# Kernel tuning notes

Measured on AMD Instinct MI355X. Metric: run time of the kernel, lower is better.

The kernel has to match this reference:

```python
import jax, jax.numpy as jnp
import numpy as np

B, N, C = 2, 2048, 768
H = 12
HD = C // H  # 64


def setup_inputs() -> dict:
    key = jax.random.key(0)
    ks = jax.random.split(key, 6)
    s = 0.02
    x = jax.random.normal(ks[0], (B, N, C), dtype=jnp.float32)
    xpos = jnp.arange(B * N, dtype=jnp.int64).reshape(B, N) % N
    W_qkv = jax.random.normal(ks[1], (3 * C, C), dtype=jnp.float32) * s
    b_qkv = jnp.zeros((3 * C,), dtype=jnp.float32)
    W_proj = jax.random.normal(ks[2], (C, C), dtype=jnp.float32) * s
    b_proj = jnp.zeros((C,), dtype=jnp.float32)
    return {"x": x, "xpos": xpos, "W_qkv": W_qkv, "b_qkv": b_qkv,
            "W_proj": W_proj, "b_proj": b_proj}


def reference(x, xpos, W_qkv, b_qkv, W_proj, b_proj):
    # rope is None in this configuration -> xpos is unused, matching torch module.
    Bx, Nx, Cx = x.shape
    scale = (Cx // H) ** -0.5
    qkv = x @ W_qkv.T + b_qkv                     # [B, N, 3C]
    qkv = qkv.reshape(Bx, Nx, 3, H, HD)
    q = jnp.einsum('bnhd->bhnd', qkv[:, :, 0])    # [B, H, N, HD]
    k = jnp.einsum('bnhd->bhnd', qkv[:, :, 1])
    v = jnp.einsum('bnhd->bhnd', qkv[:, :, 2])
    attn = jnp.einsum('bhnd,bhmd->bhnm', q, k) * scale  # [B, H, N, N]
    attn = jax.nn.softmax(attn, axis=-1)
    out = jnp.einsum('bhnm,bhmd->bhnd', attn, v)  # [B, H, N, HD]
    out = jnp.einsum('bhnd->bnhd', out).reshape(Bx, Nx, Cx)
    return out @ W_proj.T + b_proj
```

## Files before the change

kernel.cpp:

```cpp
#include <hip/hip_runtime.h>
#include <hip/hip_bf16.h>


typedef _Float16 half8 __attribute__((ext_vector_type(8)));
typedef _Float16 half4_t __attribute__((ext_vector_type(4)));
typedef float floatx4 __attribute__((ext_vector_type(4)));
typedef float floatx16 __attribute__((ext_vector_type(16)));
typedef unsigned int uintx4 __attribute__((ext_vector_type(4)));
typedef unsigned int uintx2 __attribute__((ext_vector_type(2)));

#define SCALE_LOG2E 0.1803368801111204f

constexpr int XH_OFF    = 0;
constexpr int WQKV_OFF  = XH_OFF + 4096 * 768;
constexpr int WPROJ_OFF = WQKV_OFF + 2304 * 768;
constexpr int QK_OFF    = WPROJ_OFF + 768 * 768;
constexpr int VTH_OFF   = QK_OFF + 4096 * 1536;
constexpr int PO_OFF    = VTH_OFF + 24 * 64 * 2048;
constexpr int PSTAT_OFF = PO_OFF + 2 * 24 * 2048 * 64;

__device__ __forceinline__ void gl16(const _Float16* g, _Float16* l) {
  __builtin_amdgcn_global_load_lds(
      (const __attribute__((address_space(1))) unsigned int*)g,
      (__attribute__((address_space(3))) unsigned int*)l, 16, 0, 0);
}

__global__ __launch_bounds__(256) void cvt_all(const float* __restrict__ x,
                                               const float* __restrict__ wqkv,
                                               const float* __restrict__ wproj,
                                               _Float16* __restrict__ ws) {
  constexpr int n1 = 4096 * 768 / 4;
  constexpr int n2 = 2304 * 768 / 4;
  int i = blockIdx.x * 256 + threadIdx.x;
  const float* src; _Float16* dst; int j;
  if (i < n1)           { src = x;     dst = ws + XH_OFF;    j = i; }
  else if (i < n1 + n2) { src = wqkv;  dst = ws + WQKV_OFF;  j = i - n1; }
  else                  { src = wproj; dst = ws + WPROJ_OFF; j = i - n1 - n2; }
  floatx4 f = *(const floatx4*)(src + 4 * j);
  half4_t h;
  h[0] = (_Float16)f[0]; h[1] = (_Float16)f[1];
  h[2] = (_Float16)f[2]; h[3] = (_Float16)f[3];
  *(half4_t*)(dst + 4 * j) = h;
}

__global__ __launch_bounds__(256) void qkv_gemm(const _Float16* __restrict__ xh,
                                                const _Float16* __restrict__ wh,
                                                const float* __restrict__ bias,
                                                _Float16* __restrict__ qkh,
                                                _Float16* __restrict__ vth) {
  __shared__ __align__(16) _Float16 sA[128 * 64];
  __shared__ __align__(16) _Float16 sB[128 * 64];
  const int tid = threadIdx.x;
  const int nblk = blockIdx.x % 18, mblk = blockIdx.x / 18;
  const int lane = tid & 63, w = tid >> 6;
  const int lane15 = lane & 15, quad = lane >> 4;
  const int lrow = lane >> 3, lchunk = lane & 7;
  const int wq = w >> 1, wn = w & 1;

  floatx4 acc[4][4];
#pragma unroll
  for (int mt = 0; mt < 4; ++mt)
#pragma unroll
    for (int nt = 0; nt < 4; ++nt) acc[mt][nt] = (floatx4){0.f, 0.f, 0.f, 0.f};

  for (int kt = 0; kt < 12; ++kt) {
    if (kt) __syncthreads();
#pragma unroll
    for (int i = 0; i < 8; ++i) {
      int g = i * 32 + w * 8;
      if (g < 128)
        gl16(xh + (mblk * 128 + g + lrow) * 768 + kt * 64 + lchunk * 8, sA + g * 64);
      else
        gl16(wh + (nblk * 128 + (g - 128) + lrow) * 768 + kt * 64 + lchunk * 8,
             sB + (g - 128) * 64);
    }
    __syncthreads();
#pragma unroll
    for (int ks = 0; ks < 2; ++ks) {
      half8 af[4], bf[4];
#pragma unroll
      for (int mt = 0; mt < 4; ++mt)
        af[mt] = *(const half8*)(sA + (wq * 64 + mt * 16 + lane15) * 64 + ks * 32 + quad * 8);
#pragma unroll
      for (int nt = 0; nt < 4; ++nt)
        bf[nt] = *(const half8*)(sB + (wn * 64 + nt * 16 + lane15) * 64 + ks * 32 + quad * 8);
#pragma unroll
      for (int mt = 0; mt < 4; ++mt)
#pragma unroll
        for (int nt = 0; nt < 4; ++nt)
          acc[mt][nt] = __builtin_amdgcn_mfma_f32_16x16x32_f16(af[mt], bf[nt], acc[mt][nt], 0, 0, 0);
    }
  }

  const int mbase = mblk * 128 + wq * 64;
#pragma unroll
  for (int nt = 0; nt < 4; ++nt) {
    int cbase = nblk * 128 + wn * 64 + nt * 16;
    float bv = bias[cbase + lane15];
    if (cbase < 1536) {
      int col = cbase + lane15;
      float sc = (cbase < 768) ? SCALE_LOG2E : 1.0f;
#pragma unroll
      for (int mt = 0; mt < 4; ++mt)
#pragma unroll
        for (int r = 0; r < 4; ++r) {
          int token = mbase + mt * 16 + quad * 4 + r;
          qkh[token * 1536 + col] = (_Float16)((acc[mt][nt][r] + bv) * sc);
        }
    } else {
      int dcol = cbase - 1536 + lane15;
      int h = dcol >> 6, d = dcol & 63;
#pragma unroll
      for (int mt = 0; mt < 4; ++mt) {
        int tok0 = mbase + mt * 16 + quad * 4;
        int b = tok0 >> 11, n0 = tok0 & 2047;
        int bh = b * 12 + h;
        half4_t hv;
#pragma unroll
        for (int r = 0; r < 4; ++r) hv[r] = (_Float16)(acc[mt][nt][r] + bv);
        *(half4_t*)(vth + (bh * 64 + d) * 2048 + n0) = hv;
      }
    }
  }
}

__global__ __launch_bounds__(256, 4) void attn_fused(const _Float16* __restrict__ qkh,
                                                     const _Float16* __restrict__ vth,
                                                     _Float16* __restrict__ pO,
                                                     float* __restrict__ pL) {
  __shared__ __align__(16) _Float16 sK[2][64 * 64];
  __shared__ __align__(16) _Float16 sVT[2][64 * 64];
  const int tid = threadIdx.x;
  const int bx = blockIdx.x;
  const int bh = bx % 24;
  const int rest = bx / 24;
  const int ks = rest & 1, qt = rest >> 1;
  const int b = bh / 12, h = bh % 12;
  const int lane = tid & 63, w = tid >> 6;
  const int q = lane & 31, hi = lane >> 5;

  const int qkbase = b * 2048 * 1536 + h * 64;
  const int qrow = qt * 128 + w * 32 + q;

  half8 qf[4];
#pragma unroll
  for (int c = 0; c < 4; ++c)
    qf[c] = *(const half8*)(qkh + qkbase + qrow * 1536 + c * 16 + hi * 8);

  const int l3 = lane >> 3;
  const int lc = (lane & 7) ^ l3;
  const int key0 = ks * 1024;
  const _Float16* kbase = qkh + qkbase + 768 + (key0 + w * 8 + l3) * 1536 + lc * 8;
  const _Float16* vbase = vth + (bh * 64 + w * 8 + l3) * 2048 + key0 + lc * 8;

  floatx16 O[2];
#pragma unroll
  for (int dg = 0; dg < 2; ++dg)
#pragma unroll
    for (int i = 0; i < 16; ++i) O[dg][i] = 0.f;
  float lrow = 0.f;

  auto stage = [&](int kt, int bufsel) {
    _Float16* dK = (_Float16*)sK[bufsel] + w * 512;
    _Float16* dV = (_Float16*)sVT[bufsel] + w * 512;
    const _Float16* kc = kbase + kt * 64 * 1536;
    const _Float16* vc = vbase + kt * 64;
    gl16(kc, dK);
    gl16(kc + 32 * 1536, dK + 2048);
    gl16(vc, dV);
    gl16(vc + 32 * 2048, dV + 2048);
  };

  stage(0, 0);

  for (int kt = 0; kt < 16; ++kt) {
    __syncthreads();
    if (kt < 15) stage(kt + 1, (kt + 1) & 1);
    const _Float16* cK = &sK[kt & 1][0];
    const _Float16* cV = &sVT[kt & 1][0];

    float rsum = 0.f;
#pragma unroll
    for (int og = 0; og < 2; ++og) {
      floatx16 s;
#pragma unroll
      for (int i = 0; i < 16; ++i) s[i] = 0.f;
      const int krow = og * 32 + q;
#pragma unroll
      for (int c = 0; c < 4; ++c) {
        half8 kf = *(const half8*)(cK + krow * 64 + (((c * 2 + hi) ^ (krow & 7)) * 8));
        s = __builtin_amdgcn_mfma_f32_32x32x16_f16(kf, qf[c], s, 0, 0, 0);
      }

#pragma unroll
      for (int mm = 0; mm < 2; ++mm) {
        const int rb = mm * 8;
        float e0 = __builtin_amdgcn_exp2f(s[rb + 0]);
        float e1 = __builtin_amdgcn_exp2f(s[rb + 1]);
        float e2 = __builtin_amdgcn_exp2f(s[rb + 2]);
        float e3 = __builtin_amdgcn_exp2f(s[rb + 3]);
        float e4 = __builtin_amdgcn_exp2f(s[rb + 4]);
        float e5 = __builtin_amdgcn_exp2f(s[rb + 5]);
        float e6 = __builtin_amdgcn_exp2f(s[rb + 6]);
        float e7 = __builtin_amdgcn_exp2f(s[rb + 7]);
        rsum += ((e0 + e1) + (e2 + e3)) + ((e4 + e5) + (e6 + e7));
        unsigned ua = __builtin_bit_cast(unsigned, __builtin_amdgcn_cvt_pkrtz(e0, e1));
        unsigned ub = __builtin_bit_cast(unsigned, __builtin_amdgcn_cvt_pkrtz(e2, e3));
        unsigned uc = __builtin_bit_cast(unsigned, __builtin_amdgcn_cvt_pkrtz(e4, e5));
        unsigned ud = __builtin_bit_cast(unsigned, __builtin_amdgcn_cvt_pkrtz(e6, e7));
        uintx2 sAC = __builtin_amdgcn_permlane32_swap(ua, uc, false, false);
        uintx2 sBD = __builtin_amdgcn_permlane32_swap(ub, ud, false, false);
        uintx4 u; u[0] = sAC[0]; u[1] = sBD[0]; u[2] = sAC[1]; u[3] = sBD[1];
        half8 bfrag = __builtin_bit_cast(half8, u);

        const int rc2 = (og * 2 + mm) * 2 + hi;
#pragma unroll
        for (int dg = 0; dg < 2; ++dg) {
          const int vrow = dg * 32 + q;
          half8 vf = *(const half8*)(cV + vrow * 64 + ((rc2 ^ (vrow & 7)) * 8));
          O[dg] = __builtin_amdgcn_mfma_f32_32x32x16_f16(vf, bfrag, O[dg], 0, 0, 0);
        }
      }
    }
    lrow += rsum;
  }

  const int prow = (ks * 24 + bh) * 2048 + qt * 128 + w * 32;
#pragma unroll
  for (int dg = 0; dg < 2; ++dg)
#pragma unroll
    for (int g2 = 0; g2 < 4; ++g2) {
      half4_t hv;
#pragma unroll
      for (int e = 0; e < 4; ++e) hv[e] = (_Float16)O[dg][g2 * 4 + e];
      *(half4_t*)(pO + (prow + q) * 64 + dg * 32 + g2 * 8 + hi * 4) = hv;
    }
  lrow += __shfl_xor(lrow, 32, 64);
  if (lane < 32) pL[prow + lane] = lrow;
}

__global__ __launch_bounds__(256) void proj_gemm(const _Float16* __restrict__ pO,
                                                 const float* __restrict__ pL,
                                                 const _Float16* __restrict__ wh,
                                                 const float* __restrict__ bias,
                                                 float* __restrict__ out) {
  __shared__ __align__(16) _Float16 sA[64 * 72];
  __shared__ __align__(16) _Float16 sB[128 * 64];
  const int tid = threadIdx.x;
  const int nblk = blockIdx.x % 6, mblk = blockIdx.x / 6;
  const int lane = tid & 63, w = tid >> 6;
  const int lane15 = lane & 15, quad = lane >> 4;
  const int lrow = lane >> 3, lchunk = lane & 7;
  const int arow = tid >> 2, achk = tid & 3;
  const int tok0 = mblk * 64;
  const int b = tok0 >> 11, tokl = tok0 & 2047;

  floatx4 acc[4][2];
#pragma unroll
  for (int mt = 0; mt < 4; ++mt)
#pragma unroll
    for (int nt = 0; nt < 2; ++nt) acc[mt][nt] = (floatx4){0.f, 0.f, 0.f, 0.f};

  for (int kt = 0; kt < 12; ++kt) {
    const int bh = b * 12 + kt;
    const int row1 = bh * 2048 + tokl + arow;
    const int row2 = (24 + bh) * 2048 + tokl + arow;
    float f = 1.0f / (pL[row1] + pL[row2]);

    if (kt) __syncthreads();
#pragma unroll
    for (int i = 0; i < 4; ++i) {
      int g = w * 32 + 8 * i;
      gl16(wh + (nblk * 128 + g + lrow) * 768 + kt * 64 + lchunk * 8, sB + g * 64);
    }
#pragma unroll
    for (int cc = 0; cc < 2; ++cc) {
      int c8 = achk + 4 * cc;
      half8 o1 = *(const half8*)(pO + row1 * 64 + c8 * 8);
      half8 o2 = *(const half8*)(pO + row2 * 64 + c8 * 8);
      half8 o;
#pragma unroll
      for (int e = 0; e < 8; ++e)
        o[e] = (_Float16)(f * ((float)o1[e] + (float)o2[e]));
      *(half8*)(sA + arow * 72 + c8 * 8) = o;
    }
    __syncthreads();

#pragma unroll
    for (int ksplit = 0; ksplit < 2; ++ksplit) {
      half8 af[4], bf[2];
#pragma unroll
      for (int mt = 0; mt < 4; ++mt)
        af[mt] = *(const half8*)(sA + (mt * 16 + lane15) * 72 + ksplit * 32 + quad * 8);
#pragma unroll
      for (int nt = 0; nt < 2; ++nt)
        bf[nt] = *(const half8*)(sB + (w * 32 + nt * 16 + lane15) * 64 + ksplit * 32 + quad * 8);
#pragma unroll
      for (int mt = 0; mt < 4; ++mt)
#pragma unroll
        for (int nt = 0; nt < 2; ++nt)
          acc[mt][nt] = __builtin_amdgcn_mfma_f32_16x16x32_f16(af[mt], bf[nt], acc[mt][nt], 0, 0, 0);
    }
  }

  const int mbase = mblk * 64;
#pragma unroll
  for (int nt = 0; nt < 2; ++nt) {
    int col = nblk * 128 + w * 32 + nt * 16 + lane15;
    float bv = bias[col];
#pragma unroll
    for (int mt = 0; mt < 4; ++mt)
#pragma unroll
      for (int r = 0; r < 4; ++r) {
        int token = mbase + mt * 16 + quad * 4 + r;
        out[token * 768 + col] = acc[mt][nt][r] + bv;
      }
  }
}

extern "C" void kernel_launch(void* const* d_in, const int* in_sizes, int n_in,
                              void* d_out, int out_size, void* d_ws, size_t ws_size,
                              hipStream_t stream) {
  const float* x     = (const float*)d_in[0];
  const float* wqkv  = (const float*)d_in[2];
  const float* bqkv  = (const float*)d_in[3];
  const float* wproj = (const float*)d_in[4];
  const float* bproj = (const float*)d_in[5];
  float* out = (float*)d_out;

  _Float16* ws = (_Float16*)d_ws;
  _Float16* xh     = ws + XH_OFF;
  _Float16* wqkvh  = ws + WQKV_OFF;
  _Float16* wprojh = ws + WPROJ_OFF;
  _Float16* qkh    = ws + QK_OFF;
  _Float16* vth    = ws + VTH_OFF;
  _Float16* pO     = ws + PO_OFF;
  float*    pL     = (float*)(ws + PSTAT_OFF);

  constexpr int total_v4 = (4096 * 768 + 2304 * 768 + 768 * 768) / 4;
  cvt_all<<<total_v4 / 256, 256, 0, stream>>>(x, wqkv, wproj, ws);
  qkv_gemm<<<32 * 18, 256, 0, stream>>>(xh, wqkvh, bqkv, qkh, vth);
  attn_fused<<<24 * 32, 256, 0, stream>>>(qkh, vth, pO, pL);
  proj_gemm<<<64 * 6, 256, 0, stream>>>(pO, pL, wprojh, bproj, out);
}
```

Measured before the change: 165.3 us.

## Switch QKV and projection GEMMs to 32x32x16 MFMA with XOR-swizzled LDS

Both the QKV and output-projection GEMMs now use 32x32x16 f16 MFMA tiles instead of 16x16x32, with the warp-to-tile mapping and epilogue index math rewritten to match the new accumulator layout. The LDS staging for A and B is XOR-swizzled by row, replacing the padded layout in proj, to avoid bank conflicts on the fragment reads. The aim is fewer MFMA issues and LDS reads per FLOP and conflict-free shared-memory access. It risks different register pressure and less coalesced epilogue stores.

```diff
diff --git a/kernel.cpp b/kernel.cpp
--- a/kernel.cpp
+++ b/kernel.cpp
@@ -53,15 +53,18 @@
   const int tid = threadIdx.x;
   const int nblk = blockIdx.x % 18, mblk = blockIdx.x / 18;
   const int lane = tid & 63, w = tid >> 6;
-  const int lane15 = lane & 15, quad = lane >> 4;
-  const int lrow = lane >> 3, lchunk = lane & 7;
+  const int q31 = lane & 31, hi = lane >> 5;
+  const int lrow = lane >> 3;
+  const int lchunk = (lane & 7) ^ lrow;
   const int wq = w >> 1, wn = w & 1;
 
-  floatx4 acc[4][4];
-#pragma unroll
-  for (int mt = 0; mt < 4; ++mt)
-#pragma unroll
-    for (int nt = 0; nt < 4; ++nt) acc[mt][nt] = (floatx4){0.f, 0.f, 0.f, 0.f};
+  floatx16 acc[2][2];
+#pragma unroll
+  for (int mr = 0; mr < 2; ++mr)
+#pragma unroll
+    for (int nc = 0; nc < 2; ++nc)
+#pragma unroll
+      for (int i = 0; i < 16; ++i) acc[mr][nc][i] = 0.f;
 
   for (int kt = 0; kt < 12; ++kt) {
     if (kt) __syncthreads();
@@ -76,49 +79,53 @@
     }
     __syncthreads();
 #pragma unroll
-    for (int ks = 0; ks < 2; ++ks) {
-      half8 af[4], bf[4];
-#pragma unroll
-      for (int mt = 0; mt < 4; ++mt)
-        af[mt] = *(const half8*)(sA + (wq * 64 + mt * 16 + lane15) * 64 + ks * 32 + quad * 8);
-#pragma unroll
-      for (int nt = 0; nt < 4; ++nt)
-        bf[nt] = *(const half8*)(sB + (wn * 64 + nt * 16 + lane15) * 64 + ks * 32 + quad * 8);
-#pragma unroll
-      for (int mt = 0; mt < 4; ++mt)
-#pragma unroll
-        for (int nt = 0; nt < 4; ++nt)
-          acc[mt][nt] = __builtin_amdgcn_mfma_f32_16x16x32_f16(af[mt], bf[nt], acc[mt][nt], 0, 0, 0);
-    }
-  }
-
-  const int mbase = mblk * 128 + wq * 64;
-#pragma unroll
-  for (int nt = 0; nt < 4; ++nt) {
-    int cbase = nblk * 128 + wn * 64 + nt * 16;
-    float bv = bias[cbase + lane15];
-    if (cbase < 1536) {
-      int col = cbase + lane15;
-      float sc = (cbase < 768) ? SCALE_LOG2E : 1.0f;
-#pragma unroll
-      for (int mt = 0; mt < 4; ++mt)
-#pragma unroll
-        for (int r = 0; r < 4; ++r) {
-          int token = mbase + mt * 16 + quad * 4 + r;
-          qkh[token * 1536 + col] = (_Float16)((acc[mt][nt][r] + bv) * sc);
+    for (int c = 0; c < 4; ++c) {
+      half8 af[2], bf[2];
+#pragma unroll
+      for (int mr = 0; mr < 2; ++mr) {
+        int row = wq * 64 + mr * 32 + q31;
+        af[mr] = *(const half8*)(sA + row * 64 + (((c * 2 + hi) ^ (row & 7)) * 8));
+      }
+#pragma unroll
+      for (int nc = 0; nc < 2; ++nc) {
+        int row = wn * 64 + nc * 32 + q31;
+        bf[nc] = *(const half8*)(sB + row * 64 + (((c * 2 + hi) ^ (row & 7)) * 8));
+      }
+#pragma unroll
+      for (int mr = 0; mr < 2; ++mr)
+#pragma unroll
+        for (int nc = 0; nc < 2; ++nc)
+          acc[mr][nc] = __builtin_amdgcn_mfma_f32_32x32x16_f16(af[mr], bf[nc], acc[mr][nc], 0, 0, 0);
+    }
+  }
+
+#pragma unroll
+  for (int mr = 0; mr < 2; ++mr) {
+    const int tok0 = mblk * 128 + wq * 64 + mr * 32;
+#pragma unroll
+    for (int nc = 0; nc < 2; ++nc) {
+      int cbase = nblk * 128 + wn * 64 + nc * 32;
+      int col = cbase + q31;
+      float bv = bias[col];
+      if (cbase < 1536) {
+        float sc = (cbase < 768) ? SCALE_LOG2E : 1.0f;
+#pragma unroll
+        for (int r = 0; r < 16; ++r) {
+          int token = tok0 + (r & 3) + 8 * (r >> 2) + 4 * hi;
+          qkh[token * 1536 + col] = (_Float16)((acc[mr][nc][r] + bv) * sc);
         }
-    } else {
-      int dcol = cbase - 1536 + lane15;
-      int h = dcol >> 6, d = dcol & 63;
-#pragma unroll
-      for (int mt = 0; mt < 4; ++mt) {
-        int tok0 = mbase + mt * 16 + quad * 4;
-        int b = tok0 >> 11, n0 = tok0 & 2047;
-        int bh = b * 12 + h;
-        half4_t hv;
-#pragma unroll
-        for (int r = 0; r < 4; ++r) hv[r] = (_Float16)(acc[mt][nt][r] + bv);
-        *(half4_t*)(vth + (bh * 64 + d) * 2048 + n0) = hv;
+      } else {
+        int dcol = cbase - 1536 + q31;
+        int h = dcol >> 6, d = dcol & 63;
+        int bh = (tok0 >> 11) * 12 + h;
+#pragma unroll
+        for (int g2 = 0; g2 < 4; ++g2) {
+          int n0 = (tok0 & 2047) + g2 * 8 + hi * 4;
+          half4_t hv;
+#pragma unroll
+          for (int e = 0; e < 4; ++e) hv[e] = (_Float16)(acc[mr][nc][g2 * 4 + e] + bv);
+          *(half4_t*)(vth + (bh * 64 + d) * 2048 + n0) = hv;
+        }
       }
     }
   }
@@ -244,22 +251,24 @@
                                                  const _Float16* __restrict__ wh,
                                                  const float* __restrict__ bias,
                                                  float* __restrict__ out) {
-  __shared__ __align__(16) _Float16 sA[64 * 72];
+  __shared__ __align__(16) _Float16 sA[64 * 64];
   __shared__ __align__(16) _Float16 sB[128 * 64];
   const int tid = threadIdx.x;
   const int nblk = blockIdx.x % 6, mblk = blockIdx.x / 6;
   const int lane = tid & 63, w = tid >> 6;
-  const int lane15 = lane & 15, quad = lane >> 4;
-  const int lrow = lane >> 3, lchunk = lane & 7;
+  const int q31 = lane & 31, hi = lane >> 5;
+  const int lrow = lane >> 3;
+  const int lchunk = (lane & 7) ^ lrow;
+  const int wq = w >> 1, wn = w & 1;
   const int arow = tid >> 2, achk = tid & 3;
   const int tok0 = mblk * 64;
   const int b = tok0 >> 11, tokl = tok0 & 2047;
 
-  floatx4 acc[4][2];
-#pragma unroll
-  for (int mt = 0; mt < 4; ++mt)
-#pragma unroll
-    for (int nt = 0; nt < 2; ++nt) acc[mt][nt] = (floatx4){0.f, 0.f, 0.f, 0.f};
+  floatx16 acc[2];
+#pragma unroll
+  for (int nc = 0; nc < 2; ++nc)
+#pragma unroll
+    for (int i = 0; i < 16; ++i) acc[nc][i] = 0.f;
 
   for (int kt = 0; kt < 12; ++kt) {
     const int bh = b * 12 + kt;
@@ -270,7 +279,7 @@
     if (kt) __syncthreads();
 #pragma unroll
     for (int i = 0; i < 4; ++i) {
-      int g = w * 32 + 8 * i;
+      int g = i * 32 + w * 8;
       gl16(wh + (nblk * 128 + g + lrow) * 768 + kt * 64 + lchunk * 8, sB + g * 64);
     }
 #pragma unroll
@@ -282,39 +291,36 @@
 #pragma unroll
       for (int e = 0; e < 8; ++e)
         o[e] = (_Float16)(f * ((float)o1[e] + (float)o2[e]));
-      *(half8*)(sA + arow * 72 + c8 * 8) = o;
+      *(half8*)(sA + arow * 64 + ((c8 ^ (arow & 7)) * 8)) = o;
     }
     __syncthreads();
 
 #pragma unroll
-    for (int ksplit = 0; ksplit < 2; ++ksplit) {
-      half8 af[4], bf[2];
-#pragma unroll
-      for (int mt = 0; mt < 4; ++mt)
-        af[mt] = *(const half8*)(sA + (mt * 16 + lane15) * 72 + ksplit * 32 + quad * 8);
-#pragma unroll
-      for (int nt = 0; nt < 2; ++nt)
-        bf[nt] = *(const half8*)(sB + (w * 32 + nt * 16 + lane15) * 64 + ksplit * 32 + quad * 8);
-#pragma unroll
-      for (int mt = 0; mt < 4; ++mt)
-#pragma unroll
-        for (int nt = 0; nt < 2; ++nt)
-          acc[mt][nt] = __builtin_amdgcn_mfma_f32_16x16x32_f16(af[mt], bf[nt], acc[mt][nt], 0, 0, 0);
-    }
-  }
-
-  const int mbase = mblk * 64;
-#pragma unroll
-  for (int nt = 0; nt < 2; ++nt) {
-    int col = nblk * 128 + w * 32 + nt * 16 + lane15;
+    for (int c = 0; c < 4; ++c) {
+      const int arow2 = wq * 32 + q31;
+      half8 af = *(const half8*)(sA + arow2 * 64 + (((c * 2 + hi) ^ (arow2 & 7)) * 8));
+      half8 bf[2];
+#pragma unroll
+      for (int nc = 0; nc < 2; ++nc) {
+        int row = wn * 64 + nc * 32 + q31;
+        bf[nc] = *(const half8*)(sB + row * 64 + (((c * 2 + hi) ^ (row & 7)) * 8));
+      }
+#pragma unroll
+      for (int nc = 0; nc < 2; ++nc)
+        acc[nc] = __builtin_amdgcn_mfma_f32_32x32x16_f16(af, bf[nc], acc[nc], 0, 0, 0);
+    }
+  }
+
+  const int mtok0 = mblk * 64 + wq * 32;
+#pragma unroll
+  for (int nc = 0; nc < 2; ++nc) {
+    int col = nblk * 128 + wn * 64 + nc * 32 + q31;
     float bv = bias[col];
 #pragma unroll
-    for (int mt = 0; mt < 4; ++mt)
-#pragma unroll
-      for (int r = 0; r < 4; ++r) {
-        int token = mbase + mt * 16 + quad * 4 + r;
-        out[token * 768 + col] = acc[mt][nt][r] + bv;
-      }
+    for (int r = 0; r < 16; ++r) {
+      int token = mtok0 + (r & 3) + 8 * (r >> 2) + 4 * hi;
+      out[token * 768 + col] = acc[nc][r] + bv;
+    }
   }
 }
 
```

Measured after the change: 166.7 us. No clear change (+0.8%).
